# Optimization experiments

Hardware: AMD Instinct MI355X
Metric: run time of the kernel (lower is better)

## Reference

```python
import jax, jax.numpy as jnp
import numpy as np

EMBED_DIM = 1024
NUM_HEADS = 16
HEAD_DIM = EMBED_DIM // NUM_HEADS


def setup_inputs() -> dict:
    key = jax.random.key(0)
    ks = jax.random.split(key, 9)
    s = 1.0 / np.sqrt(EMBED_DIM)
    inp = {"x": jax.random.normal(ks[0], (2, 2048, EMBED_DIM), dtype=jnp.float32)}
    for i, name in enumerate(["q", "k", "v", "out"]):
        inp[f"W_{name}"] = jax.random.uniform(ks[1 + 2 * i], (EMBED_DIM, EMBED_DIM), jnp.float32, -s, s)
        inp[f"b_{name}"] = jax.random.uniform(ks[2 + 2 * i], (EMBED_DIM,), jnp.float32, -s, s)
    return inp


def _heads(x):
    # [B, S, D] -> [B, H, S, Dh]
    b, s, _ = x.shape
    return x.reshape(b, s, NUM_HEADS, HEAD_DIM).transpose(0, 2, 1, 3)


def reference(x, W_q, b_q, W_k, b_k, W_v, b_v, W_out, b_out):
    q = _heads(x @ W_q.T + b_q)
    k = _heads(x @ W_k.T + b_k)
    v = _heads(x @ W_v.T + b_v)
    scale = HEAD_DIM ** 0.5
    logits = jnp.einsum("bhqd,bhkd->bhqk", q, k) / scale  # [B,H,S,S]
    s = x.shape[1]
    causal = jnp.tril(jnp.ones((s, s), dtype=bool))
    logits = jnp.where(causal, logits, -jnp.inf)
    a = jax.nn.softmax(logits, axis=-1)
    o = jnp.einsum("bhqk,bhkd->bhqd", a, v)
    o = o.transpose(0, 2, 1, 3).reshape(x.shape[0], s, EMBED_DIM)
    return o @ W_out.T + b_out
```

## Files before the change

kernel.cpp:

```cpp
#include <hip/hip_runtime.h>
#include <hip/hip_bf16.h>

typedef __bf16 bf16_t;
typedef __bf16 bf16x8 __attribute__((ext_vector_type(8)));
typedef __bf16 bf16x4 __attribute__((ext_vector_type(4)));
typedef float  f32x4  __attribute__((ext_vector_type(4)));

#define MFMA16(a, b, c) __builtin_amdgcn_mfma_f32_16x16x32_bf16((a), (b), (c), 0, 0, 0)

constexpr int E  = 1024;
constexpr int S  = 2048;
constexpr int H  = 16;
constexpr int M  = 4096;

__device__ __forceinline__ void glds16(const bf16_t* src, bf16_t* dst) {
  __builtin_amdgcn_global_load_lds(
      (const __attribute__((address_space(1))) void*)src,
      (__attribute__((address_space(3))) void*)dst, 16, 0, 0);
}

template <int ROWS, int NT>
__device__ __forceinline__ void stage_tile(const bf16_t* g, int gld,
                                           bf16_t* lds, int tid) {
  const int w = tid >> 6, l = tid & 63;
#pragma unroll
  for (int i = 0; i < ROWS * 8 / NT; ++i) {
    const int c = i * NT + w * 64 + l;
    const int row = c >> 3;
    const int gch = (c & 7) ^ (row & 7);
    glds16(g + (size_t)row * gld + gch * 8, lds + (size_t)(i * NT + w * 64) * 8);
  }
}

__device__ __forceinline__ bf16x8 read_frag(const bf16_t* lds, int row, int kc) {
  return *(const bf16x8*)(lds + (size_t)((row << 3) + (kc ^ (row & 7))) * 8);
}

__global__ void cvt_all_kernel(const float* __restrict__ x,
                               const float* __restrict__ w0, const float* __restrict__ w1,
                               const float* __restrict__ w2, const float* __restrict__ w3,
                               bf16_t* __restrict__ xb,
                               bf16_t* __restrict__ o0, bf16_t* __restrict__ o1,
                               bf16_t* __restrict__ o2, bf16_t* __restrict__ o3) {
  const int bid = blockIdx.x;
  const float* s;
  bf16_t* d;
  int idx;
  if (bid < 4096) {
    s = x; d = xb; idx = bid * 256 + threadIdx.x;
  } else {
    const int seg = (bid - 4096) >> 10;
    s = seg == 0 ? w0 : seg == 1 ? w1 : seg == 2 ? w2 : w3;
    d = seg == 0 ? o0 : seg == 1 ? o1 : seg == 2 ? o2 : o3;
    idx = ((bid - 4096) & 1023) * 256 + threadIdx.x;
  }
  float4 v = ((const float4*)s)[idx];
  bf16x4 o;
  o[0] = (bf16_t)v.x; o[1] = (bf16_t)v.y; o[2] = (bf16_t)v.z; o[3] = (bf16_t)v.w;
  ((bf16x4*)d)[idx] = o;
}

__device__ __forceinline__ void gemm_core(const bf16_t* __restrict__ A,
                                          const bf16_t* __restrict__ W, int Kd,
                                          bf16_t* As, bf16_t* Bs, int tid,
                                          f32x4 acc[4][4]) {
  const int w = tid >> 6, l = tid & 63;
  const int lq = l & 15, qd = l >> 4;
  const int wr = (w >> 1) * 64, wc = (w & 1) * 64;
#pragma unroll
  for (int i = 0; i < 4; ++i)
#pragma unroll
    for (int j = 0; j < 4; ++j) acc[i][j] = (f32x4){0.f, 0.f, 0.f, 0.f};

  const int KT = Kd / 64;
  for (int kt = 0; kt < KT; ++kt) {
    __syncthreads();
    stage_tile<128, 256>(A + kt * 64, Kd, As, tid);
    stage_tile<128, 256>(W + kt * 64, Kd, Bs, tid);
    __syncthreads();
#pragma unroll
    for (int ks = 0; ks < 2; ++ks) {
      bf16x8 af[4], bw[4];
#pragma unroll
      for (int mi = 0; mi < 4; ++mi)
        af[mi] = read_frag(As, wr + mi * 16 + lq, ks * 4 + qd);
#pragma unroll
      for (int ni = 0; ni < 4; ++ni)
        bw[ni] = read_frag(Bs, wc + ni * 16 + lq, ks * 4 + qd);
#pragma unroll
      for (int mi = 0; mi < 4; ++mi)
#pragma unroll
        for (int ni = 0; ni < 4; ++ni)
          acc[mi][ni] = MFMA16(af[mi], bw[ni], acc[mi][ni]);
    }
  }
}

__global__ __launch_bounds__(256) void qkv_gemm_kernel(
    const bf16_t* __restrict__ xb,
    const bf16_t* __restrict__ wq, const bf16_t* __restrict__ wk,
    const bf16_t* __restrict__ wv,
    const float* __restrict__ bq, const float* __restrict__ bk,
    const float* __restrict__ bv,
    bf16_t* __restrict__ Qb, bf16_t* __restrict__ Kb, bf16_t* __restrict__ Vb) {
  __shared__ __align__(16) bf16_t As[128 * 64];
  __shared__ __align__(16) bf16_t Bs[128 * 64];
  const int tid = threadIdx.x;
  const int which = blockIdx.x >> 3;
  const int n0 = (blockIdx.x & 7) * 128;
  const int m0 = blockIdx.y * 128;
  const bf16_t* Wp = which == 0 ? wq : which == 1 ? wk : wv;
  const float* bp  = which == 0 ? bq : which == 1 ? bk : bv;
  bf16_t* Out      = which == 0 ? Qb : which == 1 ? Kb : Vb;
  const float sc = (which == 0) ? (1.4426950408889634f * 0.125f) : 1.0f;

  f32x4 acc[4][4];
  gemm_core(xb + (size_t)m0 * E, Wp + (size_t)n0 * E, E, As, Bs, tid, acc);

  const int w = tid >> 6, l = tid & 63, lq = l & 15, qd = l >> 4;
  const int wr = (w >> 1) * 64, wc = (w & 1) * 64;
#pragma unroll
  for (int ni = 0; ni < 4; ++ni) {
    const int col = n0 + wc + ni * 16 + lq;
    const float bvv = bp[col];
#pragma unroll
    for (int mi = 0; mi < 4; ++mi)
#pragma unroll
      for (int r = 0; r < 4; ++r) {
        const int row = m0 + wr + mi * 16 + qd * 4 + r;
        Out[(size_t)row * E + col] = (bf16_t)((acc[mi][ni][r] + bvv) * sc);
      }
  }
}

__global__ __launch_bounds__(256) void vtrans_kernel(const bf16_t* __restrict__ Vb,
                                                     bf16_t* __restrict__ VT) {
  constexpr int LDT = 72;
  __shared__ __align__(16) bf16_t T[64 * LDT];
  const int tid = threadIdx.x;
  const int st = blockIdx.x, bh = blockIdx.y;
  const int b = bh >> 4, h = bh & 15;
  const int s0 = st * 64;
  const size_t rowbase = (size_t)b * S;
#pragma unroll
  for (int i = 0; i < 2; ++i) {
    const int c = i * 256 + tid;
    const int sl = c >> 3, dp = c & 7;
    const int a = sl >> 4, bb = (sl >> 2) & 3, cc = sl & 3;
    const int p = (a >> 1) * 32 + bb * 8 + (a & 1) * 4 + cc;
    bf16x8 v = *(const bf16x8*)(Vb + (rowbase + s0 + sl) * E + h * 64 + dp * 8);
    *(bf16x8*)&T[p * LDT + dp * 8] = v;
  }
  __syncthreads();
#pragma unroll
  for (int i = 0; i < 2; ++i) {
    const int c = i * 256 + tid;
    const int d = c >> 3, pp = (c & 7) * 8;
    bf16x8 o;
#pragma unroll
    for (int j = 0; j < 8; ++j) o[j] = T[(pp + j) * LDT + d];
    *(bf16x8*)&VT[((size_t)bh * 64 + d) * S + s0 + pp] = o;
  }
}

__global__ __launch_bounds__(256) void oproj_gemm_kernel(
    const bf16_t* __restrict__ Ob, const bf16_t* __restrict__ wo,
    const float* __restrict__ bo, float* __restrict__ out) {
  __shared__ __align__(16) bf16_t As[64 * 64];
  __shared__ __align__(16) bf16_t Bs[128 * 64];
  const int tid = threadIdx.x;
  const int n0 = blockIdx.x * 128;
  const int m0 = blockIdx.y * 64;
  const int w = tid >> 6, l = tid & 63, lq = l & 15, qd = l >> 4;
  const int wr = (w >> 1) * 32, wc = (w & 1) * 64;

  f32x4 acc[2][4];
#pragma unroll
  for (int i = 0; i < 2; ++i)
#pragma unroll
    for (int j = 0; j < 4; ++j) acc[i][j] = (f32x4){0.f, 0.f, 0.f, 0.f};

  for (int kt = 0; kt < 16; ++kt) {
    __syncthreads();
    stage_tile<64, 256>(Ob + (size_t)m0 * E + kt * 64, E, As, tid);
    stage_tile<128, 256>(wo + (size_t)n0 * E + kt * 64, E, Bs, tid);
    __syncthreads();
#pragma unroll
    for (int ks = 0; ks < 2; ++ks) {
      bf16x8 af[2], bw[4];
#pragma unroll
      for (int mi = 0; mi < 2; ++mi)
        af[mi] = read_frag(As, wr + mi * 16 + lq, ks * 4 + qd);
#pragma unroll
      for (int ni = 0; ni < 4; ++ni)
        bw[ni] = read_frag(Bs, wc + ni * 16 + lq, ks * 4 + qd);
#pragma unroll
      for (int mi = 0; mi < 2; ++mi)
#pragma unroll
        for (int ni = 0; ni < 4; ++ni)
          acc[mi][ni] = MFMA16(af[mi], bw[ni], acc[mi][ni]);
    }
  }
#pragma unroll
  for (int ni = 0; ni < 4; ++ni) {
    const int col = n0 + wc + ni * 16 + lq;
    const float bvv = bo[col];
#pragma unroll
    for (int mi = 0; mi < 2; ++mi)
#pragma unroll
      for (int r = 0; r < 4; ++r) {
        const int row = m0 + wr + mi * 16 + qd * 4 + r;
        out[(size_t)row * E + col] = acc[mi][ni][r] + bvv;
      }
  }
}

__global__ __launch_bounds__(256, 2) void attn_kernel(
    const bf16_t* __restrict__ Q, const bf16_t* __restrict__ K,
    const bf16_t* __restrict__ VT, bf16_t* __restrict__ O) {
  __shared__ __align__(16) bf16_t Ks[2][64 * 64];
  __shared__ __align__(16) bf16_t Vt[2][64 * 64];

  const int tid = threadIdx.x;
  const int w = tid >> 6, l = tid & 63;
  const int lq = l & 15, qd = l >> 4;
  const int bid = blockIdx.x;
  const int g = bid & 7, t = bid >> 3;
  const int bh = g * 4 + (t & 3);
  const int p = t >> 2;
  const int b = bh >> 4, h = bh & 15;
  const size_t rowbase = (size_t)b * S;
  const bf16_t* Kg = K + rowbase * E + h * 64;
  const bf16_t* Vg = VT + (size_t)bh * 64 * S;

  stage_tile<64, 256>(Kg, E, Ks[0], tid);
  stage_tile<64, 256>(Vg, S, Vt[0], tid);
  int cb = 0;

#pragma unroll 1
  for (int seg = 0; seg < 2; ++seg) {
    const int qt = seg ? p : 31 - p;
    const int qr = qt * 64 + w * 16;

    bf16x8 aq[2];
#pragma unroll
    for (int ks = 0; ks < 2; ++ks)
      aq[ks] = *(const bf16x8*)(Q + (rowbase + qr + lq) * E + h * 64 +
                                ks * 32 + qd * 8);

    f32x4 oacc[4];
#pragma unroll
    for (int nt = 0; nt < 4; ++nt) oacc[nt] = (f32x4){0.f, 0.f, 0.f, 0.f};
    float rs4[4] = {0.f, 0.f, 0.f, 0.f};

    for (int kt = 0; kt <= qt; ++kt) {
      __syncthreads();
      if (kt < qt) {
        const int kn = (kt + 1) * 64;
        stage_tile<64, 256>(Kg + (size_t)kn * E, E, Ks[cb ^ 1], tid);
        stage_tile<64, 256>(Vg + kn, S, Vt[cb ^ 1], tid);
      } else if (seg == 0) {
        stage_tile<64, 256>(Kg, E, Ks[cb ^ 1], tid);
        stage_tile<64, 256>(Vg, S, Vt[cb ^ 1], tid);
      }
      const bf16_t* Kc = Ks[cb];
      const bf16_t* Vc = Vt[cb];
      const int k0 = kt * 64;
      const bool needmask = (kt == qt);

      f32x4 sacc[4];
#pragma unroll
      for (int nt = 0; nt < 4; ++nt) sacc[nt] = (f32x4){0.f, 0.f, 0.f, 0.f};
#pragma unroll
      for (int ks = 0; ks < 2; ++ks) {
        bf16x8 bk[4];
#pragma unroll
        for (int nt = 0; nt < 4; ++nt)
          bk[nt] = read_frag(Kc, nt * 16 + lq, ks * 4 + qd);
#pragma unroll
        for (int nt = 0; nt < 4; ++nt)
          sacc[nt] = MFMA16(bk[nt], aq[ks], sacc[nt]);
      }
      bf16x8 ap[2];
#pragma unroll
      for (int nt = 0; nt < 4; ++nt)
#pragma unroll
        for (int r = 0; r < 4; ++r) {
          float pv = exp2f(sacc[nt][r]);
          if (needmask) {
            const int kg = k0 + nt * 16 + qd * 4 + r;
            const int qg = qr + lq;
            pv = (kg > qg) ? 0.f : pv;
          }
          rs4[nt] += pv;
          ap[nt >> 1][((nt & 1) << 2) | r] = (bf16_t)pv;
        }
#pragma unroll
      for (int ks = 0; ks < 2; ++ks) {
        bf16x8 bv[4];
#pragma unroll
        for (int nt = 0; nt < 4; ++nt)
          bv[nt] = read_frag(Vc, nt * 16 + lq, ks * 4 + qd);
#pragma unroll
        for (int nt = 0; nt < 4; ++nt)
          oacc[nt] = MFMA16(ap[ks], bv[nt], oacc[nt]);
      }
      cb ^= 1;
    }

    float rs = (rs4[0] + rs4[1]) + (rs4[2] + rs4[3]);
    rs += __shfl_xor(rs, 16);
    rs += __shfl_xor(rs, 32);
    float rinv[4];
#pragma unroll
    for (int r = 0; r < 4; ++r) rinv[r] = 1.0f / __shfl(rs, qd * 4 + r);
#pragma unroll
    for (int nt = 0; nt < 4; ++nt)
#pragma unroll
      for (int r = 0; r < 4; ++r) {
        const int qg = qr + qd * 4 + r;
        O[(rowbase + qg) * E + h * 64 + nt * 16 + lq] =
            (bf16_t)(oacc[nt][r] * rinv[r]);
      }
  }
}

extern "C" void kernel_launch(void* const* d_in, const int* in_sizes, int n_in,
                              void* d_out, int out_size, void* d_ws, size_t ws_size,
                              hipStream_t stream) {
  const float* x  = (const float*)d_in[0];
  const float* Wq = (const float*)d_in[1];
  const float* bq = (const float*)d_in[2];
  const float* Wk = (const float*)d_in[3];
  const float* bk = (const float*)d_in[4];
  const float* Wv = (const float*)d_in[5];
  const float* bv = (const float*)d_in[6];
  const float* Wo = (const float*)d_in[7];
  const float* bo = (const float*)d_in[8];
  float* out = (float*)d_out;

  unsigned char* ws = (unsigned char*)d_ws;
  constexpr size_t MB = 1ull << 20;
  bf16_t* xb  = (bf16_t*)(ws + 0 * MB);
  bf16_t* wqb = (bf16_t*)(ws + 8 * MB);
  bf16_t* wkb = (bf16_t*)(ws + 10 * MB);
  bf16_t* wvb = (bf16_t*)(ws + 12 * MB);
  bf16_t* wob = (bf16_t*)(ws + 14 * MB);
  bf16_t* Qb  = (bf16_t*)(ws + 16 * MB);
  bf16_t* Kb  = (bf16_t*)(ws + 24 * MB);
  bf16_t* Vb  = (bf16_t*)(ws + 32 * MB);
  bf16_t* VT  = (bf16_t*)(ws + 40 * MB);
  bf16_t* Ob  = xb;

  cvt_all_kernel<<<4096 + 4 * 1024, 256, 0, stream>>>(
      x, Wq, Wk, Wv, Wo, xb, wqb, wkb, wvb, wob);

  qkv_gemm_kernel<<<dim3(24, 32), 256, 0, stream>>>(
      xb, wqb, wkb, wvb, bq, bk, bv, Qb, Kb, Vb);

  vtrans_kernel<<<dim3(32, 32), 256, 0, stream>>>(Vb, VT);

  attn_kernel<<<512, 256, 0, stream>>>(Qb, Kb, VT, Ob);

  oproj_gemm_kernel<<<dim3(8, 64), 256, 0, stream>>>(Ob, wob, bo, out);
}
```

Measured before the change: 190.6 us.

## Rewrite QKV projection as fused 256x192-tile double-buffered GEMM with XCD-aware mapping

Replaces the three-way 128x128 QKV GEMM with one kernel over the concatenated [3072,1024] weight, using 512-thread blocks and 256x192 output tiles. The next K-tile is staged into a second LDS buffer while MFMAs run on the current one, in interleaved phases with explicit barriers, waitcnts and setprio. Block IDs are remapped so that each XCD works on a contiguous region of tiles, to improve L2 locality. The goals are to hide global-load latency and to cut sync overhead per MFMA. The cost is much higher LDS use (about 112KB per block), which limits occupancy to one block per CU.

```diff
diff --git a/kernel.cpp b/kernel.cpp
--- a/kernel.cpp
+++ b/kernel.cpp
@@ -60,75 +60,91 @@
   ((bf16x4*)d)[idx] = o;
 }
 
-__device__ __forceinline__ void gemm_core(const bf16_t* __restrict__ A,
-                                          const bf16_t* __restrict__ W, int Kd,
-                                          bf16_t* As, bf16_t* Bs, int tid,
-                                          f32x4 acc[4][4]) {
-  const int w = tid >> 6, l = tid & 63;
-  const int lq = l & 15, qd = l >> 4;
-  const int wr = (w >> 1) * 64, wc = (w & 1) * 64;
-#pragma unroll
-  for (int i = 0; i < 4; ++i)
-#pragma unroll
-    for (int j = 0; j < 4; ++j) acc[i][j] = (f32x4){0.f, 0.f, 0.f, 0.f};
-
-  const int KT = Kd / 64;
-  for (int kt = 0; kt < KT; ++kt) {
-    __syncthreads();
-    stage_tile<128, 256>(A + kt * 64, Kd, As, tid);
-    stage_tile<128, 256>(W + kt * 64, Kd, Bs, tid);
-    __syncthreads();
-#pragma unroll
-    for (int ks = 0; ks < 2; ++ks) {
-      bf16x8 af[4], bw[4];
-#pragma unroll
-      for (int mi = 0; mi < 4; ++mi)
-        af[mi] = read_frag(As, wr + mi * 16 + lq, ks * 4 + qd);
-#pragma unroll
-      for (int ni = 0; ni < 4; ++ni)
-        bw[ni] = read_frag(Bs, wc + ni * 16 + lq, ks * 4 + qd);
-#pragma unroll
-      for (int mi = 0; mi < 4; ++mi)
-#pragma unroll
-        for (int ni = 0; ni < 4; ++ni)
-          acc[mi][ni] = MFMA16(af[mi], bw[ni], acc[mi][ni]);
+__global__ __launch_bounds__(512, 2) void qkv8_kernel(
+    const bf16_t* __restrict__ xb, const bf16_t* __restrict__ W3,
+    const float* __restrict__ bq, const float* __restrict__ bk,
+    const float* __restrict__ bv, bf16_t* __restrict__ Qb) {
+  __shared__ __align__(16) bf16_t As[2][256 * 64];
+  __shared__ __align__(16) bf16_t Bs[2][192 * 64];
+  const int tid = threadIdx.x;
+  const int l = tid & 63, lq = l & 15, qd = l >> 4;
+  const int w = tid >> 6, wm = w >> 2, wn = w & 3;
+
+  const int wg = blockIdx.x;
+  const int xcd = wg & 7, i5 = wg >> 3;
+  const int region = xcd * 2 + (i5 >> 4);
+  const int j = i5 & 15;
+  const int bx = (region & 3) * 4 + (j & 3);
+  const int by = (region >> 2) * 4 + (j >> 2);
+  const int m0 = by * 256, n0 = bx * 192;
+
+  const bf16_t* Ag = xb + (size_t)m0 * E;
+  const bf16_t* Bg = W3 + (size_t)n0 * E;
+
+  f32x4 acc[8][3];
+#pragma unroll
+  for (int mi = 0; mi < 8; ++mi)
+#pragma unroll
+    for (int n = 0; n < 3; ++n) acc[mi][n] = (f32x4){0.f, 0.f, 0.f, 0.f};
+
+  stage_tile<256, 512>(Ag, E, As[0], tid);
+  stage_tile<192, 512>(Bg, E, Bs[0], tid);
+  asm volatile("s_waitcnt vmcnt(0)" ::: "memory");
+  __builtin_amdgcn_s_barrier();
+
+#pragma unroll 1
+  for (int g = 0; g < 16; ++g) {
+    const int s = g & 1;
+    const bf16_t* Al = As[s];
+    const bf16_t* Bl = Bs[s];
+    bf16_t* An = As[s ^ 1];
+    bf16_t* Bn = Bs[s ^ 1];
+    const bf16_t* Agn = Ag + (g + 1) * 64;
+    const bf16_t* Bgn = Bg + (g + 1) * 64;
+    const bool more = (g < 15);
+#pragma unroll
+    for (int q = 0; q < 4; ++q) {
+      const int mh = q >> 1, kk = q & 1;
+      bf16x8 af[4], bfr[3];
+#pragma unroll
+      for (int jj = 0; jj < 4; ++jj)
+        af[jj] = read_frag(Al, wm * 128 + (mh * 4 + jj) * 16 + lq, kk * 4 + qd);
+#pragma unroll
+      for (int n = 0; n < 3; ++n)
+        bfr[n] = read_frag(Bl, wn * 48 + n * 16 + lq, kk * 4 + qd);
+      if (more) {
+        if (q == 0) stage_tile<128, 512>(Agn, E, An, tid);
+        else if (q == 1) stage_tile<128, 512>(Agn + (size_t)128 * E, E, An + 128 * 64, tid);
+        else if (q == 2) stage_tile<192, 512>(Bgn, E, Bn, tid);
+      }
+      __builtin_amdgcn_s_barrier();
+      asm volatile("s_waitcnt lgkmcnt(0)" ::: "memory");
+      __builtin_amdgcn_sched_barrier(0);
+      __builtin_amdgcn_s_setprio(1);
+#pragma unroll
+      for (int jj = 0; jj < 4; ++jj)
+#pragma unroll
+        for (int n = 0; n < 3; ++n)
+          acc[mh * 4 + jj][n] = MFMA16(af[jj], bfr[n], acc[mh * 4 + jj][n]);
+      __builtin_amdgcn_s_setprio(0);
+      if (q == 3 && more) asm volatile("s_waitcnt vmcnt(0)" ::: "memory");
+      __builtin_amdgcn_s_barrier();
     }
   }
-}
-
-__global__ __launch_bounds__(256) void qkv_gemm_kernel(
-    const bf16_t* __restrict__ xb,
-    const bf16_t* __restrict__ wq, const bf16_t* __restrict__ wk,
-    const bf16_t* __restrict__ wv,
-    const float* __restrict__ bq, const float* __restrict__ bk,
-    const float* __restrict__ bv,
-    bf16_t* __restrict__ Qb, bf16_t* __restrict__ Kb, bf16_t* __restrict__ Vb) {
-  __shared__ __align__(16) bf16_t As[128 * 64];
-  __shared__ __align__(16) bf16_t Bs[128 * 64];
-  const int tid = threadIdx.x;
-  const int which = blockIdx.x >> 3;
-  const int n0 = (blockIdx.x & 7) * 128;
-  const int m0 = blockIdx.y * 128;
-  const bf16_t* Wp = which == 0 ? wq : which == 1 ? wk : wv;
-  const float* bp  = which == 0 ? bq : which == 1 ? bk : bv;
-  bf16_t* Out      = which == 0 ? Qb : which == 1 ? Kb : Vb;
-  const float sc = (which == 0) ? (1.4426950408889634f * 0.125f) : 1.0f;
-
-  f32x4 acc[4][4];
-  gemm_core(xb + (size_t)m0 * E, Wp + (size_t)n0 * E, E, As, Bs, tid, acc);
-
-  const int w = tid >> 6, l = tid & 63, lq = l & 15, qd = l >> 4;
-  const int wr = (w >> 1) * 64, wc = (w & 1) * 64;
-#pragma unroll
-  for (int ni = 0; ni < 4; ++ni) {
-    const int col = n0 + wc + ni * 16 + lq;
-    const float bvv = bp[col];
-#pragma unroll
-    for (int mi = 0; mi < 4; ++mi)
+
+#pragma unroll
+  for (int n = 0; n < 3; ++n) {
+    const int col = n0 + wn * 48 + n * 16 + lq;
+    const int mat = col >> 10, cc = col & 1023;
+    const float bvv = (mat == 0 ? bq : mat == 1 ? bk : bv)[cc];
+    const float sc = (mat == 0) ? 0.18033688011112043f : 1.0f;
+    bf16_t* Out = Qb + (size_t)mat * ((size_t)M * E);
+#pragma unroll
+    for (int mi = 0; mi < 8; ++mi)
 #pragma unroll
       for (int r = 0; r < 4; ++r) {
-        const int row = m0 + wr + mi * 16 + qd * 4 + r;
-        Out[(size_t)row * E + col] = (bf16_t)((acc[mi][ni][r] + bvv) * sc);
+        const int row = m0 + wm * 128 + mi * 16 + qd * 4 + r;
+        Out[(size_t)row * E + cc] = (bf16_t)((acc[mi][n][r] + bvv) * sc);
       }
   }
 }
@@ -355,8 +371,7 @@
   cvt_all_kernel<<<4096 + 4 * 1024, 256, 0, stream>>>(
       x, Wq, Wk, Wv, Wo, xb, wqb, wkb, wvb, wob);
 
-  qkv_gemm_kernel<<<dim3(24, 32), 256, 0, stream>>>(
-      xb, wqb, wkb, wvb, bq, bk, bv, Qb, Kb, Vb);
+  qkv8_kernel<<<256, 512, 0, stream>>>(xb, wqb, bq, bk, bv, Qb);
 
   vtrans_kernel<<<dim3(32, 32), 256, 0, stream>>>(Vb, VT);
 
```

Result: faster. 183.4 us (-3.8%).
